# Kernel tuning notes

Measured on AMD Instinct MI355X. Metric: run time of the kernel, lower is better.

The kernel has to match this reference:

```python
import math
import jax, jax.numpy as jnp
import numpy as np

B, S, H = 8, 1024, 1024
NH = 16
HD = H // NH  # 64


def setup_inputs() -> dict:
    key = jax.random.key(0)
    k1, k2, k3, k4 = jax.random.split(key, 4)
    hidden_states = jax.random.normal(k1, (B, S, H), dtype=jnp.float32)
    attention_mask = jax.random.randint(k2, (B, 1, 1, S), 0, 2, dtype=jnp.int32)
    w_qkv = jax.random.normal(k3, (H, 3 * H), dtype=jnp.float32) * (1.0 / math.sqrt(H))
    b_qkv = jax.random.normal(k4, (3 * H,), dtype=jnp.float32) * 0.02
    return {"hidden_states": hidden_states, "attention_mask": attention_mask,
            "w_qkv": w_qkv, "b_qkv": b_qkv}


def reference(hidden_states, attention_mask, w_qkv, b_qkv):
    b, s, _ = hidden_states.shape
    # fused QKV projection: [b, s, 3H]
    qkv = jnp.einsum('bsh,hk->bsk', hidden_states, w_qkv) + b_qkv
    # view (b, s, nh, 3*hd) -> permute -> chunk last dim (per-head q|k|v layout)
    qkv = qkv.reshape(b, s, NH, 3, HD)
    qkv = jnp.transpose(qkv, (0, 2, 1, 3, 4))      # [b, nh, s, 3, hd]
    q, k, v = qkv[..., 0, :], qkv[..., 1, :], qkv[..., 2, :]
    # raw scores, then FusedScaleMaskSoftmax semantics: scale * scores, mask, fp32 softmax
    scores = jnp.einsum('bhqd,bhkd->bhqk', q, k)
    scale = math.sqrt(HD)  # module passes sqrt(head_dim) as multiplicative scale
    scores = scores.astype(jnp.float32) * scale
    mask = attention_mask != 0                     # nonzero -> masked (padding)
    scores = jnp.where(mask, jnp.float32(-10000.0), scores)
    probs = jax.nn.softmax(scores, axis=-1).astype(hidden_states.dtype)
    # dropout prob = 0 -> identity
    context = jnp.einsum('bhqk,bhkd->bhqd', probs, v)
    context = jnp.transpose(context, (0, 2, 1, 3)).reshape(b, s, NH * HD)
    return context
```

## Files before the change

### kernel.cpp

```cpp
#include <hip/hip_runtime.h>
#include <math.h>

#define Bdim 8
#define Sdim 1024
#define Hdim 1024
#define NHd 16
#define HDd 64
#define N3H 3072

#define Q_OFF   0u
#define K_OFF   16777216u
#define V_OFF   33554432u
#define WH_OFF  41943040u
#define WL_OFF  45088768u
#define AHI_OFF 0u
#define ALO_OFF 8388608u

typedef __bf16 bf16x8 __attribute__((ext_vector_type(8)));
typedef float  f32x4  __attribute__((ext_vector_type(4)));

__device__ __forceinline__ unsigned short f2bf(float x) {
  unsigned b = __builtin_bit_cast(unsigned, x);
  return (unsigned short)((b + 0x7FFFu + ((b >> 16) & 1u)) >> 16);
}
__device__ __forceinline__ float bf2f(unsigned short h) {
  unsigned b = ((unsigned)h) << 16;
  return __builtin_bit_cast(float, b);
}
__device__ __forceinline__ void split_hl(float v, unsigned short& h, unsigned short& l) {
  h = f2bf(v);
  l = f2bf(v - bf2f(h));
}
__device__ __forceinline__ void async16(void* lds, const void* g) {
  __builtin_amdgcn_global_load_lds((const __attribute__((address_space(1))) unsigned int*)g,
                                   (__attribute__((address_space(3))) unsigned int*)lds, 16, 0, 0);
}

__global__ __launch_bounds__(256) void convert_AW(
    const float* __restrict__ A, const float* __restrict__ W,
    unsigned short* __restrict__ aout, unsigned short* __restrict__ ws)
{
  __shared__ float T[64][65];
  const int tid = threadIdx.x;
  int bid = blockIdx.x;
  if (bid < 4096) {
    size_t i = ((size_t)bid * 256 + tid) * 8;
    float4 a0 = *(const float4*)&A[i];
    float4 a1 = *(const float4*)&A[i + 4];
    float av[8] = {a0.x, a0.y, a0.z, a0.w, a1.x, a1.y, a1.z, a1.w};
    unsigned short h[8], l[8];
    #pragma unroll
    for (int j = 0; j < 8; ++j) split_hl(av[j], h[j], l[j]);
    *(uint4*)&aout[AHI_OFF + i] = *(uint4*)h;
    *(uint4*)&aout[ALO_OFF + i] = *(uint4*)l;
    return;
  }
  bid -= 4096;
  const int n0 = (bid % (N3H / 64)) * 64;
  const int k0 = (bid / (N3H / 64)) * 64;
  #pragma unroll
  for (int r = 0; r < 4; ++r) {
    int k = r * 16 + (tid >> 4);
    int n = (tid & 15) * 4;
    float4 v = *(const float4*)&W[(size_t)(k0 + k) * N3H + n0 + n];
    T[k][n + 0] = v.x; T[k][n + 1] = v.y; T[k][n + 2] = v.z; T[k][n + 3] = v.w;
  }
  __syncthreads();
  int n = tid >> 2;
  int kl = (tid & 3) * 16;
  unsigned short h[16], l[16];
  #pragma unroll
  for (int i = 0; i < 16; ++i) split_hl(T[kl + i][n], h[i], l[i]);
  size_t base = (size_t)(n0 + n) * 1024 + k0 + kl;
  *(uint4*)&ws[WH_OFF + base]     = *(uint4*)&h[0];
  *(uint4*)&ws[WH_OFF + base + 8] = *(uint4*)&h[8];
  *(uint4*)&ws[WL_OFF + base]     = *(uint4*)&l[0];
  *(uint4*)&ws[WL_OFF + base + 8] = *(uint4*)&l[8];
}

__global__ __launch_bounds__(256, 2) void qkv_mfma(
    const unsigned short* __restrict__ ao,
    const unsigned short* __restrict__ ws,
    const float* __restrict__ bias,
    unsigned short* __restrict__ wso)
{
  __shared__ unsigned short sA[2][128 * 32];
  __shared__ unsigned short sB[2][128 * 32];

  const int tid  = threadIdx.x;
  const int wave = tid >> 6;
  const int lane = tid & 63;
  const int l16  = lane & 15;
  const int quad = lane >> 4;

  const int n0 = blockIdx.x * 128;
  const int m0 = blockIdx.y * 128;
  const int wm = (wave >> 1) * 64;
  const int wn = (wave & 1) * 64;

  const unsigned short* Ah = ao + AHI_OFF;
  const unsigned short* Al = ao + ALO_OFF;
  const unsigned short* Wh = ws + WH_OFF;
  const unsigned short* Wl = ws + WL_OFF;

  f32x4 acc[4][4];
  #pragma unroll
  for (int i = 0; i < 4; ++i)
    #pragma unroll
    for (int j = 0; j < 4; ++j) acc[i][j] = (f32x4){0.f, 0.f, 0.f, 0.f};

  for (int kt = 0; kt < 1024; kt += 32) {
    __syncthreads();
    #pragma unroll
    for (int r = 0; r < 2; ++r) {
      int chunk = r * 256 + tid;
      int row = chunk >> 2;
      int c8  = (chunk & 3) << 3;
      int ldsoff = (r * 256 + wave * 64) * 8;
      async16(&sA[0][ldsoff], &Ah[(size_t)(m0 + row) * 1024 + kt + c8]);
      async16(&sA[1][ldsoff], &Al[(size_t)(m0 + row) * 1024 + kt + c8]);
      async16(&sB[0][ldsoff], &Wh[(size_t)(n0 + row) * 1024 + kt + c8]);
      async16(&sB[1][ldsoff], &Wl[(size_t)(n0 + row) * 1024 + kt + c8]);
    }
    __syncthreads();

    bf16x8 af[4][2], bf[4][2];
    #pragma unroll
    for (int i = 0; i < 4; ++i) {
      int row = wm + i * 16 + l16;
      af[i][0] = *(const bf16x8*)&sA[0][row * 32 + quad * 8];
      af[i][1] = *(const bf16x8*)&sA[1][row * 32 + quad * 8];
    }
    #pragma unroll
    for (int j = 0; j < 4; ++j) {
      int row = wn + j * 16 + l16;
      bf[j][0] = *(const bf16x8*)&sB[0][row * 32 + quad * 8];
      bf[j][1] = *(const bf16x8*)&sB[1][row * 32 + quad * 8];
    }
    #pragma unroll
    for (int i = 0; i < 4; ++i)
      #pragma unroll
      for (int j = 0; j < 4; ++j) {
        acc[i][j] = __builtin_amdgcn_mfma_f32_16x16x32_bf16(af[i][0], bf[j][0], acc[i][j], 0, 0, 0);
        acc[i][j] = __builtin_amdgcn_mfma_f32_16x16x32_bf16(af[i][1], bf[j][0], acc[i][j], 0, 0, 0);
        acc[i][j] = __builtin_amdgcn_mfma_f32_16x16x32_bf16(af[i][0], bf[j][1], acc[i][j], 0, 0, 0);
      }
  }

  const int ncol0 = n0 + wn;
  const int which = (ncol0 >> 6) % 3;
  const int head  = ncol0 / 192;
  const int mrow0 = m0 + wm;
  const int bb = mrow0 >> 10;
  const int sb = mrow0 & 1023;
  const int bh = bb * NHd + head;

  float bs[4];
  #pragma unroll
  for (int j = 0; j < 4; ++j) bs[j] = bias[ncol0 + j * 16 + l16];

  if (which == 0) {
    unsigned short* dst = wso + Q_OFF + ((size_t)bh * Sdim + sb) * 128;
    #pragma unroll
    for (int i = 0; i < 4; ++i)
      #pragma unroll
      for (int j = 0; j < 4; ++j) {
        int d = j * 16 + l16;
        #pragma unroll
        for (int r = 0; r < 4; ++r) {
          int s = i * 16 + quad * 4 + r;
          unsigned short h, l;
          split_hl(acc[i][j][r] + bs[j], h, l);
          dst[(size_t)s * 128 + d]      = h;
          dst[(size_t)s * 128 + 64 + d] = l;
        }
      }
  } else if (which == 1) {
    unsigned short* dst = wso + K_OFF + (size_t)bh * 131072 + (size_t)(sb >> 6) * 8192;
    #pragma unroll
    for (int i = 0; i < 4; ++i)
      #pragma unroll
      for (int j = 0; j < 4; ++j) {
        int c = j * 16 + l16;
        #pragma unroll
        for (int r = 0; r < 4; ++r) {
          int sp = i * 16 + quad * 4 + r;
          int idx = ((((sp >> 4) * 4 + (c >> 5)) * 64 + ((c >> 3) & 3) * 16 + (sp & 15)) << 3) + (c & 7);
          unsigned short h, l;
          split_hl(acc[i][j][r] + bs[j], h, l);
          dst[idx]        = h;
          dst[idx + 1024] = l;
        }
      }
  } else {
    unsigned short* dst = wso + V_OFF + (size_t)bh * 65536 + (size_t)(sb >> 6) * 4096;
    #pragma unroll
    for (int i = 0; i < 4; ++i)
      #pragma unroll
      for (int j = 0; j < 4; ++j) {
        int dr = j * 16 + l16;
        int ky = i * 16 + quad * 4;
        int idx = ((((dr >> 4) * 2 + (ky >> 5)) * 64 + ((ky >> 3) & 3) * 16 + (dr & 15)) << 3) + (ky & 7);
        unsigned short p[4];
        #pragma unroll
        for (int r = 0; r < 4; ++r) p[r] = f2bf(acc[i][j][r] + bs[j]);
        *(uint2*)&dst[idx] = *(uint2*)p;
      }
  }
}

__global__ __launch_bounds__(256, 4) void attn_mfma(
    const unsigned short* __restrict__ qhl,
    const unsigned short* __restrict__ khl,
    const unsigned short* __restrict__ vt,
    const int* __restrict__ mask,
    float* __restrict__ out)
{
  __shared__ unsigned short Ks[8192];
  __shared__ unsigned short Vs[4096];
  __shared__ unsigned short Pw[4][1024];
  __shared__ float msks[1024];

  const int tid  = threadIdx.x;
  const int wave = tid >> 6;
  const int lane = tid & 63;
  const int l16  = lane & 15;
  const int quad = lane >> 4;

  const int bh = blockIdx.x & 127;
  const int qt = blockIdx.x >> 7;
  const int bb = bh >> 4;
  const int q0 = qt * 64;

  const unsigned short* kplane = khl + (size_t)bh * 131072;
  const unsigned short* vplane = vt  + (size_t)bh * 65536;

  {
    int4 mv = *(const int4*)&mask[bb * Sdim + tid * 4];
    msks[tid * 4 + 0] = mv.x ? 1.f : 0.f;
    msks[tid * 4 + 1] = mv.y ? 1.f : 0.f;
    msks[tid * 4 + 2] = mv.z ? 1.f : 0.f;
    msks[tid * 4 + 3] = mv.w ? 1.f : 0.f;
  }

  bf16x8 qf[4];
  {
    int row = q0 + wave * 16 + l16;
    const unsigned short* src = qhl + ((size_t)bh * Sdim + row) * 128;
    #pragma unroll
    for (int kk = 0; kk < 4; ++kk)
      qf[kk] = *(const bf16x8*)&src[kk * 32 + quad * 8];
  }

  f32x4 O[4] = {{0.f,0.f,0.f,0.f},{0.f,0.f,0.f,0.f},{0.f,0.f,0.f,0.f},{0.f,0.f,0.f,0.f}};
  float mrow[4] = {-INFINITY, -INFINITY, -INFINITY, -INFINITY};
  float lrow[4] = {0.f, 0.f, 0.f, 0.f};

  #pragma unroll 1
  for (int kt = 0; kt < 16; ++kt) {
    __syncthreads();
    {
      const unsigned short* ksrc = kplane + (size_t)kt * 8192;
      const unsigned short* vsrc = vplane + (size_t)kt * 4096;
      #pragma unroll
      for (int r = 0; r < 4; ++r)
        async16(&Ks[(r * 256 + tid) * 8], &ksrc[(size_t)(r * 256 + tid) * 8]);
      #pragma unroll
      for (int r = 0; r < 2; ++r)
        async16(&Vs[(r * 256 + tid) * 8], &vsrc[(size_t)(r * 256 + tid) * 8]);
    }
    __syncthreads();

    f32x4 sc[4];
    #pragma unroll
    for (int ns = 0; ns < 4; ++ns) {
      f32x4 c = {0.f, 0.f, 0.f, 0.f};
      bf16x8 kf0 = *(const bf16x8*)&Ks[((ns * 4 + 0) * 64 + lane) * 8];
      bf16x8 kf1 = *(const bf16x8*)&Ks[((ns * 4 + 1) * 64 + lane) * 8];
      bf16x8 kf2 = *(const bf16x8*)&Ks[((ns * 4 + 2) * 64 + lane) * 8];
      bf16x8 kf3 = *(const bf16x8*)&Ks[((ns * 4 + 3) * 64 + lane) * 8];
      c = __builtin_amdgcn_mfma_f32_16x16x32_bf16(qf[0], kf0, c, 0, 0, 0);
      c = __builtin_amdgcn_mfma_f32_16x16x32_bf16(qf[1], kf1, c, 0, 0, 0);
      c = __builtin_amdgcn_mfma_f32_16x16x32_bf16(qf[2], kf0, c, 0, 0, 0);
      c = __builtin_amdgcn_mfma_f32_16x16x32_bf16(qf[3], kf1, c, 0, 0, 0);
      c = __builtin_amdgcn_mfma_f32_16x16x32_bf16(qf[0], kf2, c, 0, 0, 0);
      c = __builtin_amdgcn_mfma_f32_16x16x32_bf16(qf[1], kf3, c, 0, 0, 0);
      sc[ns] = c;
    }

    float rmax[4] = {-INFINITY, -INFINITY, -INFINITY, -INFINITY};
    #pragma unroll
    for (int ns = 0; ns < 4; ++ns) {
      float mk = msks[kt * 64 + ns * 16 + l16];
      #pragma unroll
      for (int r = 0; r < 4; ++r) {
        float s = (mk != 0.f) ? -10000.f : sc[ns][r] * 8.f;
        sc[ns][r] = s;
        rmax[r] = fmaxf(rmax[r], s);
      }
    }
    #pragma unroll
    for (int r = 0; r < 4; ++r) {
      float v = rmax[r];
      v = fmaxf(v, __shfl_xor(v, 1, 16));
      v = fmaxf(v, __shfl_xor(v, 2, 16));
      v = fmaxf(v, __shfl_xor(v, 4, 16));
      v = fmaxf(v, __shfl_xor(v, 8, 16));
      rmax[r] = v;
    }

    float alpha[4];
    #pragma unroll
    for (int r = 0; r < 4; ++r) {
      float mn = fmaxf(mrow[r], rmax[r]);
      alpha[r] = __expf(mrow[r] - mn);
      mrow[r] = mn;
      lrow[r] *= alpha[r];
    }
    #pragma unroll
    for (int d = 0; d < 4; ++d)
      #pragma unroll
      for (int r = 0; r < 4; ++r) O[d][r] *= alpha[r];

    float rsum[4] = {0.f, 0.f, 0.f, 0.f};
    #pragma unroll
    for (int ns = 0; ns < 4; ++ns) {
      int key = ns * 16 + l16;
      int cbase = (((key >> 5) * 4 + ((key >> 3) & 3)) * 16 + quad * 4) * 8 + (key & 7);
      #pragma unroll
      for (int r = 0; r < 4; ++r) {
        float p = __expf(sc[ns][r] - mrow[r]);
        rsum[r] += p;
        Pw[wave][cbase + r * 8] = f2bf(p);
      }
    }
    #pragma unroll
    for (int r = 0; r < 4; ++r) {
      float v = rsum[r];
      v += __shfl_xor(v, 1, 16);
      v += __shfl_xor(v, 2, 16);
      v += __shfl_xor(v, 4, 16);
      v += __shfl_xor(v, 8, 16);
      lrow[r] += v;
    }

    bf16x8 pf[2];
    #pragma unroll
    for (int kk = 0; kk < 2; ++kk)
      pf[kk] = *(const bf16x8*)&Pw[wave][((kk * 4 + quad) * 16 + l16) * 8];
    #pragma unroll
    for (int d = 0; d < 4; ++d)
      #pragma unroll
      for (int kk = 0; kk < 2; ++kk) {
        bf16x8 vf = *(const bf16x8*)&Vs[((d * 2 + kk) * 64 + lane) * 8];
        O[d] = __builtin_amdgcn_mfma_f32_16x16x32_bf16(pf[kk], vf, O[d], 0, 0, 0);
      }
  }

  const int h = bh & 15;
  #pragma unroll
  for (int r = 0; r < 4; ++r) {
    float inv = 1.f / lrow[r];
    int q = q0 + wave * 16 + quad * 4 + r;
    float* dst = out + ((size_t)bb * Sdim + q) * Hdim + h * HDd;
    #pragma unroll
    for (int d = 0; d < 4; ++d)
      dst[d * 16 + l16] = O[d][r] * inv;
  }
}

extern "C" void kernel_launch(void* const* d_in, const int* in_sizes, int n_in,
                              void* d_out, int out_size, void* d_ws, size_t ws_size,
                              hipStream_t stream) {
  const float* hs   = (const float*)d_in[0];
  const int*   mask = (const int*)d_in[1];
  const float* w    = (const float*)d_in[2];
  const float* bias = (const float*)d_in[3];
  float* out = (float*)d_out;
  unsigned short* ws = (unsigned short*)d_ws;
  unsigned short* ao = (unsigned short*)d_out;

  convert_AW<<<4096 + (N3H / 64) * (1024 / 64), 256, 0, stream>>>(hs, w, ao, ws);

  qkv_mfma<<<dim3(N3H / 128, 8192 / 128), 256, 0, stream>>>(ao, ws, bias, ws);

  attn_mfma<<<Bdim * NHd * (Sdim / 64), 256, 0, stream>>>(
      ws + Q_OFF, ws + K_OFF, ws + V_OFF, mask, out);
}
```

Before: 361.5 us.

## Pre-swizzle GEMM operands into MFMA fragment layout and skip third product for V

```diff
diff --git a/kernel.cpp b/kernel.cpp
--- a/kernel.cpp
+++ b/kernel.cpp
@@ -34,6 +34,12 @@
 __device__ __forceinline__ void async16(void* lds, const void* g) {
   __builtin_amdgcn_global_load_lds((const __attribute__((address_space(1))) unsigned int*)g,
                                    (__attribute__((address_space(3))) unsigned int*)lds, 16, 0, 0);
+}
+
+__device__ __forceinline__ size_t frag_idx(int row, int k) {
+  return ((size_t)((row >> 7) * 32 + (k >> 5)) << 12)
+       + ((size_t)((((row >> 4) & 7) * 4 + ((k >> 3) & 3)) * 16 + (row & 15)) << 3)
+       + (k & 7);
 }
 
 __global__ __launch_bounds__(256) void convert_AW(
@@ -45,14 +51,17 @@
   int bid = blockIdx.x;
   if (bid < 4096) {
     size_t i = ((size_t)bid * 256 + tid) * 8;
+    int row = (int)(i >> 10);
+    int k   = (int)(i & 1023);
     float4 a0 = *(const float4*)&A[i];
     float4 a1 = *(const float4*)&A[i + 4];
     float av[8] = {a0.x, a0.y, a0.z, a0.w, a1.x, a1.y, a1.z, a1.w};
     unsigned short h[8], l[8];
     #pragma unroll
     for (int j = 0; j < 8; ++j) split_hl(av[j], h[j], l[j]);
-    *(uint4*)&aout[AHI_OFF + i] = *(uint4*)h;
-    *(uint4*)&aout[ALO_OFF + i] = *(uint4*)l;
+    size_t dst = frag_idx(row, k);
+    *(uint4*)&aout[AHI_OFF + dst] = *(uint4*)h;
+    *(uint4*)&aout[ALO_OFF + dst] = *(uint4*)l;
     return;
   }
   bid -= 4096;
@@ -71,21 +80,22 @@
   unsigned short h[16], l[16];
   #pragma unroll
   for (int i = 0; i < 16; ++i) split_hl(T[kl + i][n], h[i], l[i]);
-  size_t base = (size_t)(n0 + n) * 1024 + k0 + kl;
-  *(uint4*)&ws[WH_OFF + base]     = *(uint4*)&h[0];
-  *(uint4*)&ws[WH_OFF + base + 8] = *(uint4*)&h[8];
-  *(uint4*)&ws[WL_OFF + base]     = *(uint4*)&l[0];
-  *(uint4*)&ws[WL_OFF + base + 8] = *(uint4*)&l[8];
-}
-
-__global__ __launch_bounds__(256, 2) void qkv_mfma(
+  size_t d0 = frag_idx(n0 + n, k0 + kl);
+  size_t d1 = frag_idx(n0 + n, k0 + kl + 8);
+  *(uint4*)&ws[WH_OFF + d0] = *(uint4*)&h[0];
+  *(uint4*)&ws[WH_OFF + d1] = *(uint4*)&h[8];
+  *(uint4*)&ws[WL_OFF + d0] = *(uint4*)&l[0];
+  *(uint4*)&ws[WL_OFF + d1] = *(uint4*)&l[8];
+}
+
+__global__ __launch_bounds__(256, 3) void qkv_mfma(
     const unsigned short* __restrict__ ao,
     const unsigned short* __restrict__ ws,
     const float* __restrict__ bias,
     unsigned short* __restrict__ wso)
 {
-  __shared__ unsigned short sA[2][128 * 32];
-  __shared__ unsigned short sB[2][128 * 32];
+  __shared__ unsigned short sA0[4096], sA1[4096];
+  __shared__ unsigned short sB0[4096], sB1[4096];
 
   const int tid  = threadIdx.x;
   const int wave = tid >> 6;
@@ -103,39 +113,43 @@
   const unsigned short* Wh = ws + WH_OFF;
   const unsigned short* Wl = ws + WL_OFF;
 
+  const int mywhich = (2 * blockIdx.x + (wave & 1)) % 3;
+  const bool needs3 = (mywhich < 2);
+
   f32x4 acc[4][4];
   #pragma unroll
   for (int i = 0; i < 4; ++i)
     #pragma unroll
     for (int j = 0; j < 4; ++j) acc[i][j] = (f32x4){0.f, 0.f, 0.f, 0.f};
 
-  for (int kt = 0; kt < 1024; kt += 32) {
+  for (int ktile = 0; ktile < 32; ++ktile) {
     __syncthreads();
-    #pragma unroll
-    for (int r = 0; r < 2; ++r) {
-      int chunk = r * 256 + tid;
-      int row = chunk >> 2;
-      int c8  = (chunk & 3) << 3;
-      int ldsoff = (r * 256 + wave * 64) * 8;
-      async16(&sA[0][ldsoff], &Ah[(size_t)(m0 + row) * 1024 + kt + c8]);
-      async16(&sA[1][ldsoff], &Al[(size_t)(m0 + row) * 1024 + kt + c8]);
-      async16(&sB[0][ldsoff], &Wh[(size_t)(n0 + row) * 1024 + kt + c8]);
-      async16(&sB[1][ldsoff], &Wl[(size_t)(n0 + row) * 1024 + kt + c8]);
+    {
+      size_t baseA = ((size_t)(blockIdx.y * 32 + ktile)) << 12;
+      size_t baseB = ((size_t)(blockIdx.x * 32 + ktile)) << 12;
+      #pragma unroll
+      for (int r = 0; r < 2; ++r) {
+        int c = r * 256 + tid;
+        async16(&sA0[c * 8], &Ah[baseA + (size_t)c * 8]);
+        async16(&sA1[c * 8], &Al[baseA + (size_t)c * 8]);
+        async16(&sB0[c * 8], &Wh[baseB + (size_t)c * 8]);
+        async16(&sB1[c * 8], &Wl[baseB + (size_t)c * 8]);
+      }
     }
     __syncthreads();
 
     bf16x8 af[4][2], bf[4][2];
     #pragma unroll
     for (int i = 0; i < 4; ++i) {
-      int row = wm + i * 16 + l16;
-      af[i][0] = *(const bf16x8*)&sA[0][row * 32 + quad * 8];
-      af[i][1] = *(const bf16x8*)&sA[1][row * 32 + quad * 8];
+      int rb = (wm >> 4) + i;
+      af[i][0] = *(const bf16x8*)&sA0[(rb * 64 + lane) * 8];
+      af[i][1] = *(const bf16x8*)&sA1[(rb * 64 + lane) * 8];
     }
     #pragma unroll
     for (int j = 0; j < 4; ++j) {
-      int row = wn + j * 16 + l16;
-      bf[j][0] = *(const bf16x8*)&sB[0][row * 32 + quad * 8];
-      bf[j][1] = *(const bf16x8*)&sB[1][row * 32 + quad * 8];
+      int rb = (wn >> 4) + j;
+      bf[j][0] = *(const bf16x8*)&sB0[(rb * 64 + lane) * 8];
+      bf[j][1] = *(const bf16x8*)&sB1[(rb * 64 + lane) * 8];
     }
     #pragma unroll
     for (int i = 0; i < 4; ++i)
@@ -143,12 +157,18 @@
       for (int j = 0; j < 4; ++j) {
         acc[i][j] = __builtin_amdgcn_mfma_f32_16x16x32_bf16(af[i][0], bf[j][0], acc[i][j], 0, 0, 0);
         acc[i][j] = __builtin_amdgcn_mfma_f32_16x16x32_bf16(af[i][1], bf[j][0], acc[i][j], 0, 0, 0);
-        acc[i][j] = __builtin_amdgcn_mfma_f32_16x16x32_bf16(af[i][0], bf[j][1], acc[i][j], 0, 0, 0);
-      }
+      }
+    if (needs3) {
+      #pragma unroll
+      for (int i = 0; i < 4; ++i)
+        #pragma unroll
+        for (int j = 0; j < 4; ++j)
+          acc[i][j] = __builtin_amdgcn_mfma_f32_16x16x32_bf16(af[i][0], bf[j][1], acc[i][j], 0, 0, 0);
+    }
   }
 
   const int ncol0 = n0 + wn;
-  const int which = (ncol0 >> 6) % 3;
+  const int which = mywhich;
   const int head  = ncol0 / 192;
   const int mrow0 = m0 + wm;
   const int bb = mrow0 >> 10;
```

After: 363.3 us. Within noise of the previous version (+0.5%).
